# Performance work log

Hardware: AMD Instinct MI355X
Metric: run time of the kernel (lower is better)

The kernel has to match this reference:

```python
import jax, jax.numpy as jnp
import numpy as np

N = 100000      # nodes
E = 1600000     # edges
IN, H, OUT = 128, 128, 64
P_DROP = 0.5


def _glorot_linear(key, out_d, in_d):
    # PyG Linear default init (kaiming-uniform-ish); exact init is irrelevant for the baseline
    bound = 1.0 / np.sqrt(in_d)
    return jax.random.uniform(key, (out_d, in_d), jnp.float32, -bound, bound)


def setup_inputs() -> dict:
    key = jax.random.key(0)
    ks = jax.random.split(key, 8)
    x = jax.random.normal(ks[0], (N, IN), jnp.float32)
    edge_index = jax.random.randint(ks[1], (2, E), 0, N, dtype=jnp.int64)
    W1l = _glorot_linear(ks[2], H, IN)
    b1 = jnp.zeros((H,), jnp.float32)
    W1r = _glorot_linear(ks[3], H, IN)
    W2l = _glorot_linear(ks[4], OUT, H)
    b2 = jnp.zeros((OUT,), jnp.float32)
    W2r = _glorot_linear(ks[5], OUT, H)
    return dict(x=x, edge_index=edge_index, W1l=W1l, b1=b1, W1r=W1r,
                W2l=W2l, b2=b2, W2r=W2r)


def _sage_conv(x, src, dst, Wl, bl, Wr):
    # PyG SAGEConv (aggr='mean'): out = lin_l(mean_{j in N(i)} x_j) + lin_r(x_i)
    msg = x[src]                                             # [E, d] gather
    agg = jax.ops.segment_sum(msg, dst, num_segments=N)      # [N, d] scatter-add
    cnt = jax.ops.segment_sum(jnp.ones((src.shape[0], 1), x.dtype), dst,
                              num_segments=N)                # [N, 1] in-degree
    mean = agg / jnp.maximum(cnt, 1.0)                       # isolated nodes -> 0
    return mean @ Wl.T + bl + x @ Wr.T


def reference(x, edge_index, W1l, b1, W1r, W2l, b2, W2r):
    src, dst = edge_index[0], edge_index[1]
    h = _sage_conv(x, src, dst, W1l, b1, W1r)
    h = jax.nn.relu(h)
    # F.dropout(p=0.5) made deterministic with a fixed key
    keep = jax.random.bernoulli(jax.random.key(42), 1.0 - P_DROP, h.shape)
    h = jnp.where(keep, h / (1.0 - P_DROP), 0.0)
    return _sage_conv(h, src, dst, W2l, b2, W2r)
```

## Files before the change

kernel.cpp:

```cpp
#include <hip/hip_runtime.h>
#include <hip/hip_bf16.h>

#define N_NODES 100000
#define NE      1600000

#define BINSH 7
#define NBIN  782
#define BCAP  3072
#define SEPB  16384
#define NBLK  ((NE + SEPB - 1) / SEPB)
#define NMASKW 200000

typedef __attribute__((ext_vector_type(8))) short bfrag;
typedef __attribute__((ext_vector_type(4))) float ffrag;

#define BFLO(u) __uint_as_float((u) << 16)
#define BFHI(u) __uint_as_float((u) & 0xffff0000u)

__device__ __forceinline__ unsigned tf_rotl(unsigned x, int d) {
    return (x << d) | (x >> (32 - d));
}

__device__ __forceinline__ unsigned tf_word(unsigned f) {
    const unsigned ks0 = 0u;
    const unsigned ks1 = 42u;
    const unsigned ks2 = 0x1BD11BDAu ^ 0u ^ 42u;
    unsigned x0 = 0u + ks0;
    unsigned x1 = f + ks1;
#define TF_RND(r) { x0 += x1; x1 = tf_rotl(x1, r); x1 ^= x0; }
    TF_RND(13) TF_RND(15) TF_RND(26) TF_RND(6)
    x0 += ks1; x1 += ks2 + 1u;
    TF_RND(17) TF_RND(29) TF_RND(16) TF_RND(24)
    x0 += ks2; x1 += ks0 + 2u;
    TF_RND(13) TF_RND(15) TF_RND(26) TF_RND(6)
    x0 += ks0; x1 += ks1 + 3u;
    TF_RND(17) TF_RND(29) TF_RND(16) TF_RND(24)
    x0 += ks1; x1 += ks2 + 4u;
    TF_RND(13) TF_RND(15) TF_RND(26) TF_RND(6)
    x0 += ks2; x1 += ks0 + 5u;
#undef TF_RND
    return x0 ^ x1;
}

__device__ __forceinline__ unsigned short bf_bits(float v) {
    __hip_bfloat16 b = __float2bfloat16(v);
    return *(unsigned short*)&b;
}

__global__ __launch_bounds__(256) void k_pre(
    const float4* __restrict__ x4, ushort4* __restrict__ xb4,
    const float* __restrict__ W1l, const float* __restrict__ W1r,
    const float* __restrict__ W2l, const float* __restrict__ W2r,
    __hip_bfloat16* __restrict__ wb,
    const int* __restrict__ ei, int* __restrict__ flag,
    int* __restrict__ bincur, unsigned long long* __restrict__ km) {
    const int tid0 = blockIdx.x * 256 + threadIdx.x;
    const int stride = gridDim.x * 256;

    for (int i = tid0; i < N_NODES * 128 / 4; i += stride) {
        float4 v = x4[i];
        ushort4 o;
        o.x = bf_bits(v.x); o.y = bf_bits(v.y);
        o.z = bf_bits(v.z); o.w = bf_bits(v.w);
        xb4[i] = o;
    }
    for (int i = tid0; i < 49152; i += stride) {
        float v;
        if (i < 16384)      v = W1l[i];
        else if (i < 32768) v = W1r[i - 16384];
        else if (i < 40960) v = W2l[i - 32768];
        else                v = W2r[i - 40960];
        wb[i] = __float2bfloat16(v);
    }
    if (blockIdx.x == 0) {
        __shared__ int nz;
        if (threadIdx.x == 0) nz = 0;
        __syncthreads();
        for (int i = threadIdx.x; i < 1024; i += 256) {
            if (ei[2 * i + 1] != 0) atomicAdd(&nz, 1);
            bincur[i] = 0;
        }
        __syncthreads();
        if (threadIdx.x == 0) *flag = (nz == 0) ? 1 : 0;
    }
    const int lane = threadIdx.x & 63;
    const int gw = tid0 >> 6;
    const int nw = stride >> 6;
    for (int widx = gw; widx < NMASKW; widx += nw) {
        unsigned wv = tf_word((unsigned)widx * 64u + (unsigned)lane);
        unsigned long long keep = __ballot(!(wv & 0x80000000u));
        if (lane == 0) km[widx] = keep;
    }
}

__global__ __launch_bounds__(1024) void k_binscatter(const int* __restrict__ ei,
        const int* __restrict__ flag, int* __restrict__ bincur,
        int* __restrict__ pairs) {
    __shared__ int h[NBIN];
    __shared__ int lbase[NBIN];
    for (int i = threadIdx.x; i < NBIN; i += 1024) h[i] = 0;
    __syncthreads();
    const int is64 = *flag;
    const int e0 = blockIdx.x * SEPB + threadIdx.x;
    int d[16], s[16];
#pragma unroll
    for (int k = 0; k < 16; ++k) {
        int e = e0 + k * 1024;
        if (e < NE) {
            d[k] = is64 ? ei[2 * (NE + e)] : ei[NE + e];
            s[k] = is64 ? ei[2 * e]        : ei[e];
            atomicAdd(&h[d[k] >> BINSH], 1);
        } else {
            d[k] = -1; s[k] = 0;
        }
    }
    __syncthreads();
    for (int i = threadIdx.x; i < NBIN; i += 1024) {
        int c = h[i];
        lbase[i] = c ? atomicAdd(&bincur[i], c) : 0;
        h[i] = 0;
    }
    __syncthreads();
#pragma unroll
    for (int k = 0; k < 16; ++k) {
        if (d[k] >= 0) {
            int b = d[k] >> BINSH;
            int r = atomicAdd(&h[b], 1);
            pairs[(size_t)b * BCAP + lbase[b] + r] =
                ((d[k] & 127) << 17) | s[k];
        }
    }
}

__global__ __launch_bounds__(256) void k_bin2csr(const int* __restrict__ pairs,
        const int* __restrict__ bincnt, int* __restrict__ ptr,
        int* __restrict__ adj) {
    __shared__ int red[256];
    __shared__ int cnt[128];
    __shared__ int sc[128];
    __shared__ int woff[128];
    const int b = blockIdx.x;
    const int t = threadIdx.x;
    int s = 0;
    for (int i = t; i < b; i += 256) s += bincnt[i];
    red[t] = s;
    __syncthreads();
    for (int o = 128; o > 0; o >>= 1) {
        if (t < o) red[t] += red[t + o];
        __syncthreads();
    }
    const int base = red[0];
    const int nb = bincnt[b];
    const int* pb = pairs + (size_t)b * BCAP;
    if (t < 128) cnt[t] = 0;
    __syncthreads();
    for (int i = t; i < nb; i += 256)
        atomicAdd(&cnt[(pb[i] >> 17) & 127], 1);
    __syncthreads();
    if (t < 128) sc[t] = cnt[t];
    __syncthreads();
    for (int o = 1; o < 128; o <<= 1) {
        int u = 0;
        if (t < 128 && t >= o) u = sc[t - o];
        __syncthreads();
        if (t < 128) sc[t] += u;
        __syncthreads();
    }
    if (t < 128) {
        int ex = sc[t] - cnt[t];
        int node = b * 128 + t;
        if (node <= N_NODES) ptr[node] = base + ex;
        woff[t] = ex;
    }
    __syncthreads();
    for (int i = t; i < nb; i += 256) {
        int pk = pb[i];
        int r = atomicAdd(&woff[(pk >> 17) & 127], 1);
        adj[base + r] = pk & 0x1FFFF;
    }
}

__global__ void k_agg(const __hip_bfloat16* __restrict__ feat,
                      const int* __restrict__ ptr, const int* __restrict__ adj,
                      __hip_bfloat16* __restrict__ mean) {
    const int wid = (blockIdx.x * blockDim.x + threadIdx.x) >> 6;
    const int lane = threadIdx.x & 63;
    if (wid >= N_NODES) return;
    const int p0 = ptr[wid], p1 = ptr[wid + 1];
    const int half = lane >> 5;
    const size_t coff = (size_t)(lane & 31) * 4;
    float c0 = 0.f, c1 = 0.f, c2 = 0.f, c3 = 0.f;
    float d0 = 0.f, d1 = 0.f, d2 = 0.f, d3 = 0.f;
    int p = p0;
    for (; p + 15 < p1; p += 16) {
        int s[8];
#pragma unroll
        for (int k = 0; k < 8; ++k) s[k] = adj[p + 2 * k + half];
#pragma unroll
        for (int k = 0; k < 8; ++k) {
            uint2 u = *(const uint2*)(feat + (size_t)s[k] * 128 + coff);
            if (k & 1) { d0 += BFLO(u.x); d1 += BFHI(u.x); d2 += BFLO(u.y); d3 += BFHI(u.y); }
            else       { c0 += BFLO(u.x); c1 += BFHI(u.x); c2 += BFLO(u.y); c3 += BFHI(u.y); }
        }
    }
    for (; p + 7 < p1; p += 8) {
        int s[4];
#pragma unroll
        for (int k = 0; k < 4; ++k) s[k] = adj[p + 2 * k + half];
#pragma unroll
        for (int k = 0; k < 4; ++k) {
            uint2 u = *(const uint2*)(feat + (size_t)s[k] * 128 + coff);
            if (k & 1) { d0 += BFLO(u.x); d1 += BFHI(u.x); d2 += BFLO(u.y); d3 += BFHI(u.y); }
            else       { c0 += BFLO(u.x); c1 += BFHI(u.x); c2 += BFLO(u.y); c3 += BFHI(u.y); }
        }
    }
    for (; p + 1 < p1; p += 2) {
        int s = adj[p + half];
        uint2 u = *(const uint2*)(feat + (size_t)s * 128 + coff);
        c0 += BFLO(u.x); c1 += BFHI(u.x); c2 += BFLO(u.y); c3 += BFHI(u.y);
    }
    if (p < p1 && half == 0) {
        int s = adj[p];
        uint2 u = *(const uint2*)(feat + (size_t)s * 128 + coff);
        c0 += BFLO(u.x); c1 += BFHI(u.x); c2 += BFLO(u.y); c3 += BFHI(u.y);
    }
    c0 += d0; c1 += d1; c2 += d2; c3 += d3;
    c0 += __shfl_xor(c0, 32);
    c1 += __shfl_xor(c1, 32);
    c2 += __shfl_xor(c2, 32);
    c3 += __shfl_xor(c3, 32);
    if (half == 0) {
        const float inv = 1.0f / (float)max(p1 - p0, 1);
        uint2 o;
        o.x = ((unsigned)bf_bits(c1 * inv) << 16) | (unsigned)bf_bits(c0 * inv);
        o.y = ((unsigned)bf_bits(c3 * inv) << 16) | (unsigned)bf_bits(c2 * inv);
        *(uint2*)(mean + (size_t)wid * 128 + coff) = o;
    }
}

__global__ __launch_bounds__(256) void k_lin1f(
    const __hip_bfloat16* __restrict__ Am, const __hip_bfloat16* __restrict__ Ax,
    const __hip_bfloat16* __restrict__ W1l, const __hip_bfloat16* __restrict__ W1r,
    const float* __restrict__ b1,
    const __hip_bfloat16* __restrict__ W2l, const __hip_bfloat16* __restrict__ W2r,
    const float* __restrict__ b2,
    const unsigned long long* __restrict__ kmask,
    __hip_bfloat16* __restrict__ y2, __hip_bfloat16* __restrict__ zb) {
    __shared__ __align__(16) __hip_bfloat16 hs[64][136];
    const int tid = threadIdx.x;
    const int w  = tid >> 6;
    const int l  = tid & 63;
    const int lr = l & 15;
    const int lk = l >> 4;
    const int j0 = w * 32;
    const int j2 = w * 16 + lr;
    const int n0 = blockIdx.x * 64;

    bfrag B1[2][2][4];
#pragma unroll
    for (int jt = 0; jt < 2; ++jt) {
        const int jrow = j0 + jt * 16 + lr;
#pragma unroll
        for (int ks = 0; ks < 4; ++ks) {
            B1[jt][0][ks] = *(const bfrag*)(W1l + jrow * 128 + ks * 32 + lk * 8);
            B1[jt][1][ks] = *(const bfrag*)(W1r + jrow * 128 + ks * 32 + lk * 8);
        }
    }
    bfrag Bl2[4], Br2[4];
#pragma unroll
    for (int ks = 0; ks < 4; ++ks) {
        Bl2[ks] = *(const bfrag*)(W2l + j2 * 128 + ks * 32 + lk * 8);
        Br2[ks] = *(const bfrag*)(W2r + j2 * 128 + ks * 32 + lk * 8);
    }
    const float bj0 = b1[j0 + lr];
    const float bj1 = b1[j0 + 16 + lr];
    const float bj2 = b2[j2];

    for (int t = 0; t < 4; ++t) {
        const int rbase = n0 + t * 16;
        int arow = rbase + lr;
        if (arow > N_NODES - 1) arow = N_NODES - 1;
        ffrag acc0 = {0.f, 0.f, 0.f, 0.f};
        ffrag acc1 = {0.f, 0.f, 0.f, 0.f};
#pragma unroll
        for (int ks = 0; ks < 4; ++ks) {
            bfrag am = *(const bfrag*)(Am + (size_t)arow * 128 + ks * 32 + lk * 8);
            bfrag ax = *(const bfrag*)(Ax + (size_t)arow * 128 + ks * 32 + lk * 8);
            acc0 = __builtin_amdgcn_mfma_f32_16x16x32_bf16(am, B1[0][0][ks], acc0, 0, 0, 0);
            acc1 = __builtin_amdgcn_mfma_f32_16x16x32_bf16(am, B1[1][0][ks], acc1, 0, 0, 0);
            acc0 = __builtin_amdgcn_mfma_f32_16x16x32_bf16(ax, B1[0][1][ks], acc0, 0, 0, 0);
            acc1 = __builtin_amdgcn_mfma_f32_16x16x32_bf16(ax, B1[1][1][ks], acc1, 0, 0, 0);
        }
#pragma unroll
        for (int r = 0; r < 4; ++r) {
            const int n = rbase + lk * 4 + r;
            const int lrow = t * 16 + lk * 4 + r;
            const int nm = (n < N_NODES) ? n : (N_NODES - 1);
            const unsigned long long km = kmask[nm * 2 + (j0 >> 6)];
            float v0 = fmaxf(acc0[r] + bj0, 0.f);
            v0 = ((km >> ((j0 + lr) & 63)) & 1ull) ? (v0 + v0) : 0.f;
            hs[lrow][j0 + lr] = __float2bfloat16(v0);
            float v1 = fmaxf(acc1[r] + bj1, 0.f);
            v1 = ((km >> ((j0 + 16 + lr) & 63)) & 1ull) ? (v1 + v1) : 0.f;
            hs[lrow][j0 + 16 + lr] = __float2bfloat16(v1);
        }
    }
    __syncthreads();

    for (int t = 0; t < 4; ++t) {
        ffrag accY = {0.f, 0.f, 0.f, 0.f};
        ffrag accZ = {0.f, 0.f, 0.f, 0.f};
#pragma unroll
        for (int ks = 0; ks < 4; ++ks) {
            bfrag ah = *(const bfrag*)&hs[t * 16 + lr][ks * 32 + lk * 8];
            accY = __builtin_amdgcn_mfma_f32_16x16x32_bf16(ah, Bl2[ks], accY, 0, 0, 0);
            accZ = __builtin_amdgcn_mfma_f32_16x16x32_bf16(ah, Br2[ks], accZ, 0, 0, 0);
        }
#pragma unroll
        for (int r = 0; r < 4; ++r) {
            const int n = n0 + t * 16 + lk * 4 + r;
            if (n < N_NODES) {
                y2[(size_t)n * 64 + j2] = __float2bfloat16(accY[r]);
                zb[(size_t)n * 64 + j2] = __float2bfloat16(accZ[r] + bj2);
            }
        }
    }
}

__global__ void k_agg2f(const __hip_bfloat16* __restrict__ feat,
                        const int* __restrict__ ptr, const int* __restrict__ adj,
                        const __hip_bfloat16* __restrict__ zb,
                        float* __restrict__ out) {
    const int node = (blockIdx.x * blockDim.x + threadIdx.x) >> 5;
    const int sl = threadIdx.x & 31;
    if (node >= N_NODES) return;
    const int p0 = ptr[node], p1 = ptr[node + 1];
    const int sub = sl >> 4;
    const size_t coff = (size_t)(sl & 15) * 4;
    float c0 = 0.f, c1 = 0.f, c2 = 0.f, c3 = 0.f;
    float d0 = 0.f, d1 = 0.f, d2 = 0.f, d3 = 0.f;
    int p = p0;
    for (; p + 15 < p1; p += 16) {
        int s[8];
#pragma unroll
        for (int k = 0; k < 8; ++k) s[k] = adj[p + 2 * k + sub];
#pragma unroll
        for (int k = 0; k < 8; ++k) {
            uint2 u = *(const uint2*)(feat + (size_t)s[k] * 64 + coff);
            if (k & 1) { d0 += BFLO(u.x); d1 += BFHI(u.x); d2 += BFLO(u.y); d3 += BFHI(u.y); }
            else       { c0 += BFLO(u.x); c1 += BFHI(u.x); c2 += BFLO(u.y); c3 += BFHI(u.y); }
        }
    }
    for (; p + 7 < p1; p += 8) {
        int s[4];
#pragma unroll
        for (int k = 0; k < 4; ++k) s[k] = adj[p + 2 * k + sub];
#pragma unroll
        for (int k = 0; k < 4; ++k) {
            uint2 u = *(const uint2*)(feat + (size_t)s[k] * 64 + coff);
            if (k & 1) { d0 += BFLO(u.x); d1 += BFHI(u.x); d2 += BFLO(u.y); d3 += BFHI(u.y); }
            else       { c0 += BFLO(u.x); c1 += BFHI(u.x); c2 += BFLO(u.y); c3 += BFHI(u.y); }
        }
    }
    for (; p + 1 < p1; p += 2) {
        int s = adj[p + sub];
        uint2 u = *(const uint2*)(feat + (size_t)s * 64 + coff);
        c0 += BFLO(u.x); c1 += BFHI(u.x); c2 += BFLO(u.y); c3 += BFHI(u.y);
    }
    if (p < p1 && sub == 0) {
        int s = adj[p];
        uint2 u = *(const uint2*)(feat + (size_t)s * 64 + coff);
        c0 += BFLO(u.x); c1 += BFHI(u.x); c2 += BFLO(u.y); c3 += BFHI(u.y);
    }
    c0 += d0; c1 += d1; c2 += d2; c3 += d3;
    c0 += __shfl_xor(c0, 16);
    c1 += __shfl_xor(c1, 16);
    c2 += __shfl_xor(c2, 16);
    c3 += __shfl_xor(c3, 16);
    if (sub == 0) {
        const float inv = 1.0f / (float)max(p1 - p0, 1);
        uint2 zu = *(const uint2*)(zb + (size_t)node * 64 + coff);
        float4 o;
        o.x = BFLO(zu.x) + c0 * inv;
        o.y = BFHI(zu.x) + c1 * inv;
        o.z = BFLO(zu.y) + c2 * inv;
        o.w = BFHI(zu.y) + c3 * inv;
        *(float4*)(out + (size_t)node * 64 + coff) = o;
    }
}

extern "C" void kernel_launch(void* const* d_in, const int* in_sizes, int n_in,
                              void* d_out, int out_size, void* d_ws, size_t ws_size,
                              hipStream_t stream) {
    const float* x   = (const float*)d_in[0];
    const int*   ei  = (const int*)d_in[1];
    const float* W1l = (const float*)d_in[2];
    const float* b1  = (const float*)d_in[3];
    const float* W1r = (const float*)d_in[4];
    const float* W2l = (const float*)d_in[5];
    const float* b2  = (const float*)d_in[6];
    const float* W2r = (const float*)d_in[7];
    float* out = (float*)d_out;

    char* w = (char*)d_ws;
    int* flag   = (int*)w;
    int* bincur = flag + 64;
    int* ptr    = bincur + 1024;
    int* adj    = ptr + (N_NODES + 1);
    size_t koff = (((size_t)(64 + 1024 + N_NODES + 1 + NE)) * 4 + 255)
                  & ~(size_t)255;
    unsigned long long* kmask = (unsigned long long*)(w + koff);
    size_t foff = (koff + (size_t)NMASKW * 8 + 255) & ~(size_t)255;
    __hip_bfloat16* wb    = (__hip_bfloat16*)(w + foff);
    __hip_bfloat16* w1lb  = wb;
    __hip_bfloat16* w1rb  = wb + 16384;
    __hip_bfloat16* w2lb  = wb + 32768;
    __hip_bfloat16* w2rb  = wb + 40960;
    __hip_bfloat16* xb    = wb + 49152;
    __hip_bfloat16* meanb = xb + (size_t)N_NODES * 128;
    char* pregion = (char*)(meanb + (size_t)N_NODES * 128);
    int* pairs = (int*)pregion;
    __hip_bfloat16* y2b = (__hip_bfloat16*)pregion;
    __hip_bfloat16* zbb = y2b + (size_t)N_NODES * 64;

    k_pre<<<2048, 256, 0, stream>>>((const float4*)x, (ushort4*)xb,
                                    W1l, W1r, W2l, W2r, wb,
                                    ei, flag, bincur, kmask);

    k_binscatter<<<NBLK, 1024, 0, stream>>>(ei, flag, bincur, pairs);
    k_bin2csr<<<NBIN, 256, 0, stream>>>(pairs, bincur, ptr, adj);

    const int ab  = (N_NODES + 3) / 4;
    const int nb  = (N_NODES + 63) / 64;
    const int ab2 = (N_NODES + 7) / 8;

    k_agg<<<ab, 256, 0, stream>>>(xb, ptr, adj, meanb);
    k_lin1f<<<nb, 256, 0, stream>>>(meanb, xb, w1lb, w1rb, b1,
                                    w2lb, w2rb, b2, kmask, y2b, zbb);
    k_agg2f<<<ab2, 256, 0, stream>>>(y2b, ptr, adj, zbb, out);
}
```

Measured before the change: 233.2 us.

## Fuse layer-1 neighbor aggregation into the linear kernel via shared memory

Merges the separate mean-aggregation kernel into the first linear kernel. Each block now gathers neighbor means for its 64 nodes straight into LDS and feeds them to the MFMA tiles, so the intermediate mean buffer is never written to or re-read from global memory. The trade-off is a less parallel gather phase, with each wave handling 16 nodes in sequence inside a 256-thread block instead of one node per wave. The fused kernel also holds more registers, which could lower occupancy and latency hiding for the random gathers.

```diff
diff --git a/kernel.cpp b/kernel.cpp
--- a/kernel.cpp
+++ b/kernel.cpp
@@ -180,81 +180,84 @@
     }
 }
 
-__global__ void k_agg(const __hip_bfloat16* __restrict__ feat,
-                      const int* __restrict__ ptr, const int* __restrict__ adj,
-                      __hip_bfloat16* __restrict__ mean) {
-    const int wid = (blockIdx.x * blockDim.x + threadIdx.x) >> 6;
-    const int lane = threadIdx.x & 63;
-    if (wid >= N_NODES) return;
-    const int p0 = ptr[wid], p1 = ptr[wid + 1];
-    const int half = lane >> 5;
-    const size_t coff = (size_t)(lane & 31) * 4;
-    float c0 = 0.f, c1 = 0.f, c2 = 0.f, c3 = 0.f;
-    float d0 = 0.f, d1 = 0.f, d2 = 0.f, d3 = 0.f;
-    int p = p0;
-    for (; p + 15 < p1; p += 16) {
-        int s[8];
-#pragma unroll
-        for (int k = 0; k < 8; ++k) s[k] = adj[p + 2 * k + half];
-#pragma unroll
-        for (int k = 0; k < 8; ++k) {
-            uint2 u = *(const uint2*)(feat + (size_t)s[k] * 128 + coff);
-            if (k & 1) { d0 += BFLO(u.x); d1 += BFHI(u.x); d2 += BFLO(u.y); d3 += BFHI(u.y); }
-            else       { c0 += BFLO(u.x); c1 += BFHI(u.x); c2 += BFLO(u.y); c3 += BFHI(u.y); }
-        }
-    }
-    for (; p + 7 < p1; p += 8) {
-        int s[4];
-#pragma unroll
-        for (int k = 0; k < 4; ++k) s[k] = adj[p + 2 * k + half];
-#pragma unroll
-        for (int k = 0; k < 4; ++k) {
-            uint2 u = *(const uint2*)(feat + (size_t)s[k] * 128 + coff);
-            if (k & 1) { d0 += BFLO(u.x); d1 += BFHI(u.x); d2 += BFLO(u.y); d3 += BFHI(u.y); }
-            else       { c0 += BFLO(u.x); c1 += BFHI(u.x); c2 += BFLO(u.y); c3 += BFHI(u.y); }
-        }
-    }
-    for (; p + 1 < p1; p += 2) {
-        int s = adj[p + half];
-        uint2 u = *(const uint2*)(feat + (size_t)s * 128 + coff);
-        c0 += BFLO(u.x); c1 += BFHI(u.x); c2 += BFLO(u.y); c3 += BFHI(u.y);
-    }
-    if (p < p1 && half == 0) {
-        int s = adj[p];
-        uint2 u = *(const uint2*)(feat + (size_t)s * 128 + coff);
-        c0 += BFLO(u.x); c1 += BFHI(u.x); c2 += BFLO(u.y); c3 += BFHI(u.y);
-    }
-    c0 += d0; c1 += d1; c2 += d2; c3 += d3;
-    c0 += __shfl_xor(c0, 32);
-    c1 += __shfl_xor(c1, 32);
-    c2 += __shfl_xor(c2, 32);
-    c3 += __shfl_xor(c3, 32);
-    if (half == 0) {
-        const float inv = 1.0f / (float)max(p1 - p0, 1);
-        uint2 o;
-        o.x = ((unsigned)bf_bits(c1 * inv) << 16) | (unsigned)bf_bits(c0 * inv);
-        o.y = ((unsigned)bf_bits(c3 * inv) << 16) | (unsigned)bf_bits(c2 * inv);
-        *(uint2*)(mean + (size_t)wid * 128 + coff) = o;
-    }
-}
-
-__global__ __launch_bounds__(256) void k_lin1f(
-    const __hip_bfloat16* __restrict__ Am, const __hip_bfloat16* __restrict__ Ax,
+__global__ __launch_bounds__(256) void k_agglin(
+    const __hip_bfloat16* __restrict__ feat,
+    const int* __restrict__ ptr, const int* __restrict__ adj,
     const __hip_bfloat16* __restrict__ W1l, const __hip_bfloat16* __restrict__ W1r,
     const float* __restrict__ b1,
     const __hip_bfloat16* __restrict__ W2l, const __hip_bfloat16* __restrict__ W2r,
     const float* __restrict__ b2,
     const unsigned long long* __restrict__ kmask,
     __hip_bfloat16* __restrict__ y2, __hip_bfloat16* __restrict__ zb) {
-    __shared__ __align__(16) __hip_bfloat16 hs[64][136];
+    __shared__ __align__(16) __hip_bfloat16 sh[64][136];
     const int tid = threadIdx.x;
     const int w  = tid >> 6;
     const int l  = tid & 63;
+    const int n0 = blockIdx.x * 64;
+
+    {
+        const int half = l >> 5;
+        const size_t coff = (size_t)(l & 31) * 4;
+        for (int i = 0; i < 16; ++i) {
+            const int row = w * 16 + i;
+            int node = n0 + row;
+            if (node > N_NODES - 1) node = N_NODES - 1;
+            const int p0 = ptr[node], p1 = ptr[node + 1];
+            float c0 = 0.f, c1 = 0.f, c2 = 0.f, c3 = 0.f;
+            float d0 = 0.f, d1 = 0.f, d2 = 0.f, d3 = 0.f;
+            int p = p0;
+            for (; p + 15 < p1; p += 16) {
+                int s[8];
+#pragma unroll
+                for (int k = 0; k < 8; ++k) s[k] = adj[p + 2 * k + half];
+#pragma unroll
+                for (int k = 0; k < 8; ++k) {
+                    uint2 u = *(const uint2*)(feat + (size_t)s[k] * 128 + coff);
+                    if (k & 1) { d0 += BFLO(u.x); d1 += BFHI(u.x); d2 += BFLO(u.y); d3 += BFHI(u.y); }
+                    else       { c0 += BFLO(u.x); c1 += BFHI(u.x); c2 += BFLO(u.y); c3 += BFHI(u.y); }
+                }
+            }
+            for (; p + 7 < p1; p += 8) {
+                int s[4];
+#pragma unroll
+                for (int k = 0; k < 4; ++k) s[k] = adj[p + 2 * k + half];
+#pragma unroll
+                for (int k = 0; k < 4; ++k) {
+                    uint2 u = *(const uint2*)(feat + (size_t)s[k] * 128 + coff);
+                    if (k & 1) { d0 += BFLO(u.x); d1 += BFHI(u.x); d2 += BFLO(u.y); d3 += BFHI(u.y); }
+                    else       { c0 += BFLO(u.x); c1 += BFHI(u.x); c2 += BFLO(u.y); c3 += BFHI(u.y); }
+                }
+            }
+            for (; p + 1 < p1; p += 2) {
+                int s = adj[p + half];
+                uint2 u = *(const uint2*)(feat + (size_t)s * 128 + coff);
+                c0 += BFLO(u.x); c1 += BFHI(u.x); c2 += BFLO(u.y); c3 += BFHI(u.y);
+            }
+            if (p < p1 && half == 0) {
+                int s = adj[p];
+                uint2 u = *(const uint2*)(feat + (size_t)s * 128 + coff);
+                c0 += BFLO(u.x); c1 += BFHI(u.x); c2 += BFLO(u.y); c3 += BFHI(u.y);
+            }
+            c0 += d0; c1 += d1; c2 += d2; c3 += d3;
+            c0 += __shfl_xor(c0, 32);
+            c1 += __shfl_xor(c1, 32);
+            c2 += __shfl_xor(c2, 32);
+            c3 += __shfl_xor(c3, 32);
+            if (half == 0) {
+                const float inv = 1.0f / (float)max(p1 - p0, 1);
+                uint2 o;
+                o.x = ((unsigned)bf_bits(c1 * inv) << 16) | (unsigned)bf_bits(c0 * inv);
+                o.y = ((unsigned)bf_bits(c3 * inv) << 16) | (unsigned)bf_bits(c2 * inv);
+                *(uint2*)&sh[row][(l & 31) * 4] = o;
+            }
+        }
+    }
+    __syncthreads();
+
     const int lr = l & 15;
     const int lk = l >> 4;
     const int j0 = w * 32;
     const int j2 = w * 16 + lr;
-    const int n0 = blockIdx.x * 64;
 
     bfrag B1[2][2][4];
 #pragma unroll
@@ -266,53 +269,60 @@
             B1[jt][1][ks] = *(const bfrag*)(W1r + jrow * 128 + ks * 32 + lk * 8);
         }
     }
-    bfrag Bl2[4], Br2[4];
-#pragma unroll
-    for (int ks = 0; ks < 4; ++ks) {
-        Bl2[ks] = *(const bfrag*)(W2l + j2 * 128 + ks * 32 + lk * 8);
-        Br2[ks] = *(const bfrag*)(W2r + j2 * 128 + ks * 32 + lk * 8);
-    }
     const float bj0 = b1[j0 + lr];
     const float bj1 = b1[j0 + 16 + lr];
-    const float bj2 = b2[j2];
-
+
+    ffrag acc0[4], acc1[4];
+#pragma unroll
     for (int t = 0; t < 4; ++t) {
         const int rbase = n0 + t * 16;
         int arow = rbase + lr;
         if (arow > N_NODES - 1) arow = N_NODES - 1;
-        ffrag acc0 = {0.f, 0.f, 0.f, 0.f};
-        ffrag acc1 = {0.f, 0.f, 0.f, 0.f};
+        acc0[t] = (ffrag){0.f, 0.f, 0.f, 0.f};
+        acc1[t] = (ffrag){0.f, 0.f, 0.f, 0.f};
 #pragma unroll
         for (int ks = 0; ks < 4; ++ks) {
-            bfrag am = *(const bfrag*)(Am + (size_t)arow * 128 + ks * 32 + lk * 8);
-            bfrag ax = *(const bfrag*)(Ax + (size_t)arow * 128 + ks * 32 + lk * 8);
-            acc0 = __builtin_amdgcn_mfma_f32_16x16x32_bf16(am, B1[0][0][ks], acc0, 0, 0, 0);
-            acc1 = __builtin_amdgcn_mfma_f32_16x16x32_bf16(am, B1[1][0][ks], acc1, 0, 0, 0);
-            acc0 = __builtin_amdgcn_mfma_f32_16x16x32_bf16(ax, B1[0][1][ks], acc0, 0, 0, 0);
-            acc1 = __builtin_amdgcn_mfma_f32_16x16x32_bf16(ax, B1[1][1][ks], acc1, 0, 0, 0);
-        }
+            bfrag am = *(const bfrag*)&sh[t * 16 + lr][ks * 32 + lk * 8];
+            bfrag ax = *(const bfrag*)(feat + (size_t)arow * 128 + ks * 32 + lk * 8);
+            acc0[t] = __builtin_amdgcn_mfma_f32_16x16x32_bf16(am, B1[0][0][ks], acc0[t], 0, 0, 0);
+            acc1[t] = __builtin_amdgcn_mfma_f32_16x16x32_bf16(am, B1[1][0][ks], acc1[t], 0, 0, 0);
+            acc0[t] = __builtin_amdgcn_mfma_f32_16x16x32_bf16(ax, B1[0][1][ks], acc0[t], 0, 0, 0);
+            acc1[t] = __builtin_amdgcn_mfma_f32_16x16x32_bf16(ax, B1[1][1][ks], acc1[t], 0, 0, 0);
+        }
+    }
+    __syncthreads();
+
+#pragma unroll
+    for (int t = 0; t < 4; ++t) {
 #pragma unroll
         for (int r = 0; r < 4; ++r) {
-            const int n = rbase + lk * 4 + r;
+            const int n = n0 + t * 16 + lk * 4 + r;
             const int lrow = t * 16 + lk * 4 + r;
             const int nm = (n < N_NODES) ? n : (N_NODES - 1);
             const unsigned long long km = kmask[nm * 2 + (j0 >> 6)];
-            float v0 = fmaxf(acc0[r] + bj0, 0.f);
+            float v0 = fmaxf(acc0[t][r] + bj0, 0.f);
             v0 = ((km >> ((j0 + lr) & 63)) & 1ull) ? (v0 + v0) : 0.f;
-            hs[lrow][j0 + lr] = __float2bfloat16(v0);
-            float v1 = fmaxf(acc1[r] + bj1, 0.f);
+            sh[lrow][j0 + lr] = __float2bfloat16(v0);
+            float v1 = fmaxf(acc1[t][r] + bj1, 0.f);
             v1 = ((km >> ((j0 + 16 + lr) & 63)) & 1ull) ? (v1 + v1) : 0.f;
-            hs[lrow][j0 + 16 + lr] = __float2bfloat16(v1);
-        }
-    }
-    __syncthreads();
-
+            sh[lrow][j0 + 16 + lr] = __float2bfloat16(v1);
+        }
+    }
+    __syncthreads();
+
+    bfrag Bl2[4], Br2[4];
+#pragma unroll
+    for (int ks = 0; ks < 4; ++ks) {
+        Bl2[ks] = *(const bfrag*)(W2l + j2 * 128 + ks * 32 + lk * 8);
+        Br2[ks] = *(const bfrag*)(W2r + j2 * 128 + ks * 32 + lk * 8);
+    }
+    const float bj2 = b2[j2];
     for (int t = 0; t < 4; ++t) {
         ffrag accY = {0.f, 0.f, 0.f, 0.f};
         ffrag accZ = {0.f, 0.f, 0.f, 0.f};
 #pragma unroll
         for (int ks = 0; ks < 4; ++ks) {
-            bfrag ah = *(const bfrag*)&hs[t * 16 + lr][ks * 32 + lk * 8];
+            bfrag ah = *(const bfrag*)&sh[t * 16 + lr][ks * 32 + lk * 8];
             accY = __builtin_amdgcn_mfma_f32_16x16x32_bf16(ah, Bl2[ks], accY, 0, 0, 0);
             accZ = __builtin_amdgcn_mfma_f32_16x16x32_bf16(ah, Br2[ks], accZ, 0, 0, 0);
         }
@@ -417,8 +427,7 @@
     __hip_bfloat16* w2lb  = wb + 32768;
     __hip_bfloat16* w2rb  = wb + 40960;
     __hip_bfloat16* xb    = wb + 49152;
-    __hip_bfloat16* meanb = xb + (size_t)N_NODES * 128;
-    char* pregion = (char*)(meanb + (size_t)N_NODES * 128);
+    char* pregion = (char*)(xb + (size_t)N_NODES * 128);
     int* pairs = (int*)pregion;
     __hip_bfloat16* y2b = (__hip_bfloat16*)pregion;
     __hip_bfloat16* zbb = y2b + (size_t)N_NODES * 64;
@@ -430,12 +439,10 @@
     k_binscatter<<<NBLK, 1024, 0, stream>>>(ei, flag, bincur, pairs);
     k_bin2csr<<<NBIN, 256, 0, stream>>>(pairs, bincur, ptr, adj);
 
-    const int ab  = (N_NODES + 3) / 4;
     const int nb  = (N_NODES + 63) / 64;
     const int ab2 = (N_NODES + 7) / 8;
 
-    k_agg<<<ab, 256, 0, stream>>>(xb, ptr, adj, meanb);
-    k_lin1f<<<nb, 256, 0, stream>>>(meanb, xb, w1lb, w1rb, b1,
-                                    w2lb, w2rb, b2, kmask, y2b, zbb);
+    k_agglin<<<nb, 256, 0, stream>>>(xb, ptr, adj, w1lb, w1rb, b1,
+                                     w2lb, w2rb, b2, kmask, y2b, zbb);
     k_agg2f<<<ab2, 256, 0, stream>>>(y2b, ptr, adj, zbb, out);
 }
```

Measured after the change: 276.1 us. +18.4%, slower.

## Fuse CSR construction with first-layer neighbor aggregation using shared-memory adjacency

Applied to the files above, without the earlier changes.

Merges the bin-to-CSR kernel and the first mean-aggregation kernel into one 1024-thread block per bin. Each block stages its bin's adjacency in LDS and then aggregates its 128 nodes directly from it. This removes a launch and the global re-read of ptr/adj for layer one. In exchange each wave processes 8 nodes serially and the grid shrinks to one block per bin, which may reduce memory-level parallelism for the gather.

```diff
diff --git a/kernel.cpp b/kernel.cpp
--- a/kernel.cpp
+++ b/kernel.cpp
@@ -132,29 +132,39 @@
     }
 }
 
-__global__ __launch_bounds__(256) void k_bin2csr(const int* __restrict__ pairs,
-        const int* __restrict__ bincnt, int* __restrict__ ptr,
-        int* __restrict__ adj) {
-    __shared__ int red[256];
+__global__ __launch_bounds__(1024) void k_aggcsr(
+        const __hip_bfloat16* __restrict__ feat,
+        const int* __restrict__ pairs, const int* __restrict__ bincnt,
+        int* __restrict__ ptr, int* __restrict__ adj,
+        __hip_bfloat16* __restrict__ mean) {
+    __shared__ int ladj[BCAP];
     __shared__ int cnt[128];
     __shared__ int sc[128];
     __shared__ int woff[128];
+    __shared__ int red[16];
+    __shared__ int base_s;
     const int b = blockIdx.x;
     const int t = threadIdx.x;
+
     int s = 0;
-    for (int i = t; i < b; i += 256) s += bincnt[i];
-    red[t] = s;
-    __syncthreads();
-    for (int o = 128; o > 0; o >>= 1) {
-        if (t < o) red[t] += red[t + o];
-        __syncthreads();
-    }
-    const int base = red[0];
+    for (int i = t; i < b; i += 1024) s += bincnt[i];
+#pragma unroll
+    for (int off = 32; off > 0; off >>= 1) s += __shfl_down(s, off);
+    if ((t & 63) == 0) red[t >> 6] = s;
+    if (t < 128) cnt[t] = 0;
+    __syncthreads();
+    if (t == 0) {
+        int tot = 0;
+#pragma unroll
+        for (int i = 0; i < 16; ++i) tot += red[i];
+        base_s = tot;
+    }
+    __syncthreads();
+    const int base = base_s;
     const int nb = bincnt[b];
     const int* pb = pairs + (size_t)b * BCAP;
-    if (t < 128) cnt[t] = 0;
-    __syncthreads();
-    for (int i = t; i < nb; i += 256)
+
+    for (int i = t; i < nb; i += 1024)
         atomicAdd(&cnt[(pb[i] >> 17) & 127], 1);
     __syncthreads();
     if (t < 128) sc[t] = cnt[t];
@@ -173,68 +183,72 @@
         woff[t] = ex;
     }
     __syncthreads();
-    for (int i = t; i < nb; i += 256) {
+    for (int i = t; i < nb; i += 1024) {
         int pk = pb[i];
         int r = atomicAdd(&woff[(pk >> 17) & 127], 1);
-        adj[base + r] = pk & 0x1FFFF;
-    }
-}
-
-__global__ void k_agg(const __hip_bfloat16* __restrict__ feat,
-                      const int* __restrict__ ptr, const int* __restrict__ adj,
-                      __hip_bfloat16* __restrict__ mean) {
-    const int wid = (blockIdx.x * blockDim.x + threadIdx.x) >> 6;
-    const int lane = threadIdx.x & 63;
-    if (wid >= N_NODES) return;
-    const int p0 = ptr[wid], p1 = ptr[wid + 1];
-    const int half = lane >> 5;
-    const size_t coff = (size_t)(lane & 31) * 4;
-    float c0 = 0.f, c1 = 0.f, c2 = 0.f, c3 = 0.f;
-    float d0 = 0.f, d1 = 0.f, d2 = 0.f, d3 = 0.f;
-    int p = p0;
-    for (; p + 15 < p1; p += 16) {
-        int s[8];
-#pragma unroll
-        for (int k = 0; k < 8; ++k) s[k] = adj[p + 2 * k + half];
-#pragma unroll
-        for (int k = 0; k < 8; ++k) {
-            uint2 u = *(const uint2*)(feat + (size_t)s[k] * 128 + coff);
-            if (k & 1) { d0 += BFLO(u.x); d1 += BFHI(u.x); d2 += BFLO(u.y); d3 += BFHI(u.y); }
-            else       { c0 += BFLO(u.x); c1 += BFHI(u.x); c2 += BFLO(u.y); c3 += BFHI(u.y); }
-        }
-    }
-    for (; p + 7 < p1; p += 8) {
-        int s[4];
-#pragma unroll
-        for (int k = 0; k < 4; ++k) s[k] = adj[p + 2 * k + half];
-#pragma unroll
-        for (int k = 0; k < 4; ++k) {
-            uint2 u = *(const uint2*)(feat + (size_t)s[k] * 128 + coff);
-            if (k & 1) { d0 += BFLO(u.x); d1 += BFHI(u.x); d2 += BFLO(u.y); d3 += BFHI(u.y); }
-            else       { c0 += BFLO(u.x); c1 += BFHI(u.x); c2 += BFLO(u.y); c3 += BFHI(u.y); }
-        }
-    }
-    for (; p + 1 < p1; p += 2) {
-        int s = adj[p + half];
-        uint2 u = *(const uint2*)(feat + (size_t)s * 128 + coff);
-        c0 += BFLO(u.x); c1 += BFHI(u.x); c2 += BFLO(u.y); c3 += BFHI(u.y);
-    }
-    if (p < p1 && half == 0) {
-        int s = adj[p];
-        uint2 u = *(const uint2*)(feat + (size_t)s * 128 + coff);
-        c0 += BFLO(u.x); c1 += BFHI(u.x); c2 += BFLO(u.y); c3 += BFHI(u.y);
-    }
-    c0 += d0; c1 += d1; c2 += d2; c3 += d3;
-    c0 += __shfl_xor(c0, 32);
-    c1 += __shfl_xor(c1, 32);
-    c2 += __shfl_xor(c2, 32);
-    c3 += __shfl_xor(c3, 32);
-    if (half == 0) {
-        const float inv = 1.0f / (float)max(p1 - p0, 1);
-        uint2 o;
-        o.x = ((unsigned)bf_bits(c1 * inv) << 16) | (unsigned)bf_bits(c0 * inv);
-        o.y = ((unsigned)bf_bits(c3 * inv) << 16) | (unsigned)bf_bits(c2 * inv);
-        *(uint2*)(mean + (size_t)wid * 128 + coff) = o;
+        int src = pk & 0x1FFFF;
+        ladj[r] = src;
+        adj[base + r] = src;
+    }
+    __syncthreads();
+
+    const int w = t >> 6;
+    const int l = t & 63;
+    const int half = l >> 5;
+    const size_t coff = (size_t)(l & 31) * 4;
+    for (int i = 0; i < 8; ++i) {
+        const int local = w * 8 + i;
+        const int node = b * 128 + local;
+        if (node >= N_NODES) continue;
+        const int p1 = sc[local];
+        const int p0 = p1 - cnt[local];
+        float c0 = 0.f, c1 = 0.f, c2 = 0.f, c3 = 0.f;
+        float d0 = 0.f, d1 = 0.f, d2 = 0.f, d3 = 0.f;
+        int p = p0;
+        for (; p + 15 < p1; p += 16) {
+            int sx[8];
+#pragma unroll
+            for (int k = 0; k < 8; ++k) sx[k] = ladj[p + 2 * k + half];
+#pragma unroll
+            for (int k = 0; k < 8; ++k) {
+                uint2 u = *(const uint2*)(feat + (size_t)sx[k] * 128 + coff);
+                if (k & 1) { d0 += BFLO(u.x); d1 += BFHI(u.x); d2 += BFLO(u.y); d3 += BFHI(u.y); }
+                else       { c0 += BFLO(u.x); c1 += BFHI(u.x); c2 += BFLO(u.y); c3 += BFHI(u.y); }
+            }
+        }
+        for (; p + 7 < p1; p += 8) {
+            int sx[4];
+#pragma unroll
+            for (int k = 0; k < 4; ++k) sx[k] = ladj[p + 2 * k + half];
+#pragma unroll
+            for (int k = 0; k < 4; ++k) {
+                uint2 u = *(const uint2*)(feat + (size_t)sx[k] * 128 + coff);
+                if (k & 1) { d0 += BFLO(u.x); d1 += BFHI(u.x); d2 += BFLO(u.y); d3 += BFHI(u.y); }
+                else       { c0 += BFLO(u.x); c1 += BFHI(u.x); c2 += BFLO(u.y); c3 += BFHI(u.y); }
+            }
+        }
+        for (; p + 1 < p1; p += 2) {
+            int sx = ladj[p + half];
+            uint2 u = *(const uint2*)(feat + (size_t)sx * 128 + coff);
+            c0 += BFLO(u.x); c1 += BFHI(u.x); c2 += BFLO(u.y); c3 += BFHI(u.y);
+        }
+        if (p < p1 && half == 0) {
+            int sx = ladj[p];
+            uint2 u = *(const uint2*)(feat + (size_t)sx * 128 + coff);
+            c0 += BFLO(u.x); c1 += BFHI(u.x); c2 += BFLO(u.y); c3 += BFHI(u.y);
+        }
+        c0 += d0; c1 += d1; c2 += d2; c3 += d3;
+        c0 += __shfl_xor(c0, 32);
+        c1 += __shfl_xor(c1, 32);
+        c2 += __shfl_xor(c2, 32);
+        c3 += __shfl_xor(c3, 32);
+        if (half == 0) {
+            const float inv = 1.0f / (float)max(p1 - p0, 1);
+            uint2 o;
+            o.x = ((unsigned)bf_bits(c1 * inv) << 16) | (unsigned)bf_bits(c0 * inv);
+            o.y = ((unsigned)bf_bits(c3 * inv) << 16) | (unsigned)bf_bits(c2 * inv);
+            *(uint2*)(mean + (size_t)node * 128 + coff) = o;
+        }
     }
 }
 
@@ -428,13 +442,12 @@
                                     ei, flag, bincur, kmask);
 
     k_binscatter<<<NBLK, 1024, 0, stream>>>(ei, flag, bincur, pairs);
-    k_bin2csr<<<NBIN, 256, 0, stream>>>(pairs, bincur, ptr, adj);
-
-    const int ab  = (N_NODES + 3) / 4;
+
+    k_aggcsr<<<NBIN, 1024, 0, stream>>>(xb, pairs, bincur, ptr, adj, meanb);
+
     const int nb  = (N_NODES + 63) / 64;
     const int ab2 = (N_NODES + 7) / 8;
 
-    k_agg<<<ab, 256, 0, stream>>>(xb, ptr, adj, meanb);
     k_lin1f<<<nb, 256, 0, stream>>>(meanb, xb, w1lb, w1rb, b1,
                                     w2lb, w2rb, b2, kmask, y2b, zbb);
     k_agg2f<<<ab2, 256, 0, stream>>>(y2b, ptr, adj, zbb, out);
```

Result: no change. 231.1 us (-0.9%).
